# Kernel optimization log

Hardware: AMD Instinct MI355X
Metric: run time of the kernel (lower is better)

## Reference

```python
import jax, jax.numpy as jnp
import numpy as np
from jax import lax

DN = ('NCHW', 'OIHW', 'NCHW')

def conv(x, w, b, stride=1, pad=0):
    y = lax.conv_general_dilated(x, w, (stride, stride), ((pad, pad), (pad, pad)), dimension_numbers=DN)
    return y + b[None, :, None, None]

def conv_transpose(x, w, b):
    # torch ConvTranspose2d(k=4, s=2, p=1): w is (in_ch, out_ch, 4, 4)
    wf = jnp.flip(w, (2, 3)).transpose(1, 0, 2, 3)  # -> (out_ch, in_ch, 4, 4)
    pad = 4 - 1 - 1  # k - 1 - p = 2
    y = lax.conv_general_dilated(x, wf, (1, 1), ((pad, pad), (pad, pad)), lhs_dilation=(2, 2), dimension_numbers=DN)
    return y + b[None, :, None, None]

def setup_inputs() -> dict:
    key = jax.random.key(0)
    ks = jax.random.split(key, 16)
    HID, ZC, K = 256, 64, 512
    def w(k, shape):
        return (jax.random.normal(k, shape, jnp.float32) * 0.02)
    z = lambda n: jnp.zeros((n,), jnp.float32)
    return {
        'x': jax.random.uniform(ks[0], (8, 3, 128, 128), jnp.float32),
        'c1_w': w(ks[1], (HID, 3, 4, 4)), 'c1_b': z(HID),
        'c2_w': w(ks[2], (HID, HID, 4, 4)), 'c2_b': z(HID),
        'r0_w3': w(ks[3], (HID, HID, 3, 3)), 'r0_b3': z(HID),
        'r0_w1': w(ks[4], (HID, HID, 1, 1)), 'r0_b1': z(HID),
        'r1_w3': w(ks[5], (HID, HID, 3, 3)), 'r1_b3': z(HID),
        'r1_w1': w(ks[6], (HID, HID, 1, 1)), 'r1_b1': z(HID),
        'to_z_w': w(ks[7], (ZC, HID, 1, 1)), 'to_z_b': z(ZC),
        'codebook': jax.random.uniform(ks[8], (K, ZC), jnp.float32, -1.0 / K, 1.0 / K),
        'from_z_w': w(ks[9], (HID, ZC, 1, 1)), 'from_z_b': z(HID),
        't1_w': w(ks[10], (HID, HID, 4, 4)), 't1_b': z(HID),
        't2_w': w(ks[11], (HID, 3, 4, 4)), 't2_b': z(3),
    }

def _vqvae(x, c1_w, c1_b, c2_w, c2_b, r0_w3, r0_b3, r0_w1, r0_b1,
           r1_w3, r1_b3, r1_w1, r1_b1, to_z_w, to_z_b, codebook,
           from_z_w, from_z_b, t1_w, t1_b, t2_w, t2_b):
    # ---- Encoder ----
    h = jax.nn.relu(conv(x, c1_w, c1_b, stride=2, pad=1))
    h = jax.nn.relu(conv(h, c2_w, c2_b, stride=2, pad=1))
    for (w3, b3, w1, b1) in ((r0_w3, r0_b3, r0_w1, r0_b1), (r1_w3, r1_b3, r1_w1, r1_b1)):
        r = conv(jax.nn.relu(h), w3, b3, pad=1)
        r = conv(jax.nn.relu(r), w1, b1)
        h = h + r
    z_e = conv(h, to_z_w, to_z_b)  # [B, ZC, H/4, W/4]
    # ---- Vector quantization ----
    B, C, H, W = z_e.shape
    z_flat = z_e.transpose(0, 2, 3, 1).reshape(-1, C)  # [N, C]
    dist = (jnp.sum(z_flat * z_flat, axis=1, keepdims=True)
            - 2.0 * z_flat @ codebook.T
            + jnp.sum(codebook * codebook, axis=1)[None, :])  # [N, K]
    ids = jnp.argmin(dist, axis=1)  # [N]
    e_k_flat = codebook[ids]  # [N, C]
    e_k_st_flat = z_flat + lax.stop_gradient(e_k_flat - z_flat)
    e_k = e_k_flat.reshape(B, H, W, C).transpose(0, 3, 1, 2)
    e_k_st = e_k_st_flat.reshape(B, H, W, C).transpose(0, 3, 1, 2)
    ids = ids.reshape(B, H, W)
    # ---- Decoder ----
    d = jax.nn.relu(conv(e_k_st, from_z_w, from_z_b))
    d = jax.nn.relu(conv_transpose(d, t1_w, t1_b))
    out = jax.nn.sigmoid(conv_transpose(d, t2_w, t2_b))
    return out, z_e, e_k, ids

def reference(x, c1_w, c1_b, c2_w, c2_b, r0_w3, r0_b3, r0_w1, r0_b1,
              r1_w3, r1_b3, r1_w1, r1_b1, to_z_w, to_z_b, codebook,
              from_z_w, from_z_b, t1_w, t1_b, t2_w, t2_b):
    return _vqvae(x, c1_w, c1_b, c2_w, c2_b, r0_w3, r0_b3, r0_w1, r0_b1,
                  r1_w3, r1_b3, r1_w1, r1_b1, to_z_w, to_z_b, codebook,
                  from_z_w, from_z_b, t1_w, t1_b, t2_w, t2_b)
```

## Files before the change

kernel.cpp:

```cpp
#include <hip/hip_runtime.h>
#include <math.h>


typedef unsigned int uint;
typedef unsigned short ushort_t;
using short8 = __attribute__((ext_vector_type(8))) short;
using f32x4  = __attribute__((ext_vector_type(4))) float;

__device__ __attribute__((aligned(16))) ushort_t g_zpad[512];

static __device__ __forceinline__ int rfl(int x) { return __builtin_amdgcn_readfirstlane(x); }
static __device__ __forceinline__ ushort_t f2bf(float f) {
  uint u = __float_as_uint(f);
  return (ushort_t)((u + 0x7fffu + ((u >> 16) & 1u)) >> 16);
}
static __device__ __forceinline__ float bf2f(ushort_t b) {
  return __uint_as_float(((uint)b) << 16);
}
static __device__ __forceinline__ void gload16(const ushort_t* g, void* l) {
  __builtin_amdgcn_global_load_lds(
      (const __attribute__((address_space(1))) void*)g,
      (__attribute__((address_space(3))) void*)l, 16, 0, 0);
}

__global__ __launch_bounds__(256) void k_prep_misc(
    const float* __restrict__ c1w, float* __restrict__ wt_c1,
    const float* __restrict__ tozw, float* __restrict__ wt_toz,
    const float* __restrict__ fromzw, float* __restrict__ wt_fromz,
    const float* __restrict__ cb, float* __restrict__ cnorm,
    const float* __restrict__ t2w, ushort_t* __restrict__ w2pk)
{
  const int b = blockIdx.x, tid = threadIdx.x;
  if (b < 48) {
    int idx = b * 256 + tid;
    int co = idx % 256, i = idx / 256;
    wt_c1[idx] = c1w[co * 48 + i];
  } else if (b < 112) {
    int idx = (b - 48) * 256 + tid;
    int co = idx % 64, i = idx / 64;
    wt_toz[idx] = tozw[co * 256 + i];
  } else if (b < 176) {
    int idx = (b - 112) * 256 + tid;
    int co = idx % 256, i = idx / 256;
    wt_fromz[idx] = fromzw[co * 64 + i];
  } else if (b < 178) {
    int idx = (b - 176) * 256 + tid;
    if (idx < 512) {
      float s = 0.f;
      for (int c = 0; c < 64; ++c) { float v = cb[idx * 64 + c]; s = fmaf(v, v, s); }
      cnorm[idx] = s;
    }
  } else {
    int idx = (b - 178) * 256 + tid;
    int k = idx & 31, co = (idx >> 5) & 15, chunk = (idx >> 9) & 31, par = idx >> 14;
    int tap = chunk >> 3, cg = chunk & 7;
    int a = tap >> 1, bb = tap & 1;
    int ry = par & 1, rx = (par >> 1) & 1;
    int ky = ((ry + 1) & 1) + 2 * a;
    int kx = ((rx + 1) & 1) + 2 * bb;
    int ci = cg * 32 + k;
    float v = (co < 3) ? t2w[((ci * 3 + co) << 4) + ky * 4 + kx] : 0.f;
    w2pk[idx] = f2bf(v);
  }
}

template<int KIND>
__global__ __launch_bounds__(256) void k_prep_enc(
    const float* __restrict__ w, ushort_t* __restrict__ wp)
{
  constexpr int KK = (KIND == 0) ? 16 : (KIND == 1 ? 9 : 1);
  constexpr int KW = (KIND == 0) ? 4  : (KIND == 1 ? 3 : 1);
  constexpr int NT = KK;
  const int tid = threadIdx.x;
  const int wvg = blockIdx.x * 4 + (tid >> 6);
  const int lane = tid & 63;
  const int co = wvg >> 2;
  const int ci = (wvg & 3) * 64 + lane;
  const float* src = w + (size_t)(co * 256 + ci) * KK;
  const int coT = co >> 6, row = co & 63, cg = ci >> 5, k = ci & 31;
  float v[KK];
#pragma unroll
  for (int j = 0; j < KK; ++j) v[j] = src[j];
#pragma unroll
  for (int tap = 0; tap < NT; ++tap) {
    int ky, kx;
    if (KIND == 0)      { ky = tap >> 2; kx = tap & 3; }
    else if (KIND == 1) { ky = tap / 3;  kx = tap - ky * 3; }
    else                { ky = 0; kx = 0; }
    float val = v[ky * KW + kx];
    ushort_t b0 = f2bf(val);
    ushort_t b1 = f2bf(val - bf2f(b0));
    const int chunk = tap * 8 + cg;
    size_t base = ((size_t)(chunk * 4 + coT) << 12) + row * 32 + k;
    wp[base] = b0;
    wp[base + 2048] = b1;
  }
}

template<int KIND>
__global__ __launch_bounds__(256) void k_prep_enc2(
    const float* __restrict__ wa, ushort_t* __restrict__ oa,
    const float* __restrict__ wb2, ushort_t* __restrict__ ob)
{
  constexpr int KK = (KIND == 0) ? 16 : (KIND == 1 ? 9 : 1);
  constexpr int KW = (KIND == 0) ? 4  : (KIND == 1 ? 3 : 1);
  constexpr int NT = KK;
  const float* w = (blockIdx.x < 256) ? wa : wb2;
  ushort_t* wp = (blockIdx.x < 256) ? oa : ob;
  const int bx = blockIdx.x & 255;
  const int tid = threadIdx.x;
  const int wvg = bx * 4 + (tid >> 6);
  const int lane = tid & 63;
  const int co = wvg >> 2;
  const int ci = (wvg & 3) * 64 + lane;
  const float* src = w + (size_t)(co * 256 + ci) * KK;
  const int coT = co >> 6, row = co & 63, cg = ci >> 5, k = ci & 31;
  float v[KK];
#pragma unroll
  for (int j = 0; j < KK; ++j) v[j] = src[j];
#pragma unroll
  for (int tap = 0; tap < NT; ++tap) {
    int ky, kx;
    if (KIND == 0)      { ky = tap >> 2; kx = tap & 3; }
    else if (KIND == 1) { ky = tap / 3;  kx = tap - ky * 3; }
    else                { ky = 0; kx = 0; }
    float val = v[ky * KW + kx];
    ushort_t b0 = f2bf(val);
    ushort_t b1 = f2bf(val - bf2f(b0));
    const int chunk = tap * 8 + cg;
    size_t base = ((size_t)(chunk * 4 + coT) << 12) + row * 32 + k;
    wp[base] = b0;
    wp[base + 2048] = b1;
  }
}

__global__ void k_prep_t1w(const float* __restrict__ w, ushort_t* __restrict__ wb) {
  int idx = blockIdx.x * 256 + threadIdx.x;
  int kk  = idx & 31;
  int co  = (idx >> 5) & 255;
  int c8  = (idx >> 13) & 7;
  int tap = (idx >> 16) & 3;
  int par = idx >> 18;
  int ry = par & 1, rx = (par >> 1) & 1;
  int a = tap >> 1, b = tap & 1;
  int ky = ((ry + 1) & 1) + 2 * a;
  int kx = ((rx + 1) & 1) + 2 * b;
  int ci = c8 * 32 + kk;
  wb[idx] = f2bf(w[((ci * 256 + co) << 4) + ky * 4 + kx]);
}

__global__ __launch_bounds__(256) void k_conv1_split(
    const float* __restrict__ in, ushort_t* __restrict__ o0, ushort_t* __restrict__ o1,
    const float* __restrict__ wT, const float* __restrict__ bias)
{
  __shared__ float s_in[3 * 360];
  const int tid = threadIdx.x;
  const int lane = tid & 63;
  const int wv = rfl(tid >> 6);
  const int px = lane & 7, py = lane >> 3;
  const int tx = blockIdx.x & 7, ty = blockIdx.x >> 3;
  const int X = tx * 8, Y = ty * 8;
  const int cob = blockIdx.y * 64 + wv * 16;
  const int n = blockIdx.z;
  float acc[16];
#pragma unroll
  for (int i = 0; i < 16; ++i) acc[i] = bias[cob + i];
  const float* inN = in + (size_t)n * 3 * 16384;
  for (int e = tid; e < 3 * 360; e += 256) {
    int col2 = e % 20; int t = e / 20; int row = t % 18; int ci = t / 18;
    int pr = col2 / 10, hc = col2 % 10, ixl = 2 * hc + pr;
    int iy = 2 * Y - 1 + row, ix = 2 * X - 1 + ixl;
    float v = 0.f;
    if (ixl < 18 && (unsigned)iy < 128u && (unsigned)ix < 128u)
      v = inN[ci * 16384 + iy * 128 + ix];
    s_in[e] = v;
  }
  __syncthreads();
  const float* wc = wT + cob;
#pragma unroll
  for (int c = 0; c < 3; ++c) {
    const float* base = s_in + c * 360 + py * 40 + px;
#pragma unroll
    for (int ky = 0; ky < 4; ++ky) {
#pragma unroll
      for (int kx = 0; kx < 4; ++kx) {
        float iv = base[ky * 20 + (kx & 1) * 10 + (kx >> 1)];
        const float* w = wc + (size_t)(c * 16 + ky * 4 + kx) * 256;
#pragma unroll
        for (int i = 0; i < 16; ++i) acc[i] = fmaf(iv, w[i], acc[i]);
      }
    }
  }
  const int pxg = n * 4096 + (Y + py) * 64 + (X + px);
  uint p0[8], p1[8];
#pragma unroll
  for (int i = 0; i < 8; ++i) {
    float va = fmaxf(acc[2 * i], 0.f), vb = fmaxf(acc[2 * i + 1], 0.f);
    ushort_t a0 = f2bf(va), b0 = f2bf(vb);
    ushort_t a1 = f2bf(va - bf2f(a0)), b1 = f2bf(vb - bf2f(b0));
    p0[i] = (uint)a0 | ((uint)b0 << 16);
    p1[i] = (uint)a1 | ((uint)b1 << 16);
  }
  ushort_t* d0 = o0 + (size_t)pxg * 256 + cob;
  ushort_t* d1 = o1 + (size_t)pxg * 256 + cob;
  uint4 v0a; v0a.x = p0[0]; v0a.y = p0[1]; v0a.z = p0[2]; v0a.w = p0[3];
  uint4 v0b; v0b.x = p0[4]; v0b.y = p0[5]; v0b.z = p0[6]; v0b.w = p0[7];
  uint4 v1a; v1a.x = p1[0]; v1a.y = p1[1]; v1a.z = p1[2]; v1a.w = p1[3];
  uint4 v1b; v1b.x = p1[4]; v1b.y = p1[5]; v1b.z = p1[6]; v1b.w = p1[7];
  *(uint4*)d0 = v0a; *(uint4*)(d0 + 8) = v0b;
  *(uint4*)d1 = v1a; *(uint4*)(d1 + 8) = v1b;
}

template<int KIND>
__global__ __launch_bounds__(256) void k_enc_mfma_split(
    const ushort_t* __restrict__ x0, const ushort_t* __restrict__ x1,
    const ushort_t* __restrict__ wp, float* __restrict__ part)
{
  __shared__ ushort_t smem[2][12288];
  const int tid = threadIdx.x, lane = tid & 63, wv = tid >> 6;
  const int l15 = lane & 15, q = lane >> 4;
  const int pxT = blockIdx.x, coT = blockIdx.y;
  constexpr int NCH = (KIND == 0) ? 128 : 72;
  const int CH0 = blockIdx.z * (NCH / 2), CH1 = CH0 + NCH / 2;
  f32x4 acc[4][2];
#pragma unroll
  for (int m = 0; m < 4; ++m)
#pragma unroll
    for (int n = 0; n < 2; ++n) acc[m][n] = (f32x4){0.f, 0.f, 0.f, 0.f};

  const int r0 = tid >> 2, kq = tid & 3;
  int bimg[2], bu[2], bvc[2];
#pragma unroll
  for (int r = 0; r < 2; ++r) {
    int bpx = pxT * 128 + r0 + r * 64;
    bimg[r] = bpx >> 10; int bp = bpx & 1023; bu[r] = bp >> 5; bvc[r] = bp & 31;
  }
  const ushort_t* srcB[2][2];
  int ptap = -1;
  auto retap = [&](int tap) {
    ptap = tap;
    int ky, kx;
    if (KIND == 0) { ky = tap >> 2; kx = tap & 3; }
    else           { ky = tap / 3;  kx = tap - ky * 3; }
#pragma unroll
    for (int r = 0; r < 2; ++r) {
      bool v; size_t rowb;
      if (KIND == 0) {
        int iy = 2 * bu[r] - 1 + ky, ix = 2 * bvc[r] - 1 + kx;
        v = ((unsigned)iy < 64u) && ((unsigned)ix < 64u);
        rowb = ((size_t)(bimg[r] * 4096 + iy * 64 + ix)) << 8;
      } else {
        int iy = bu[r] - 1 + ky, ix = bvc[r] - 1 + kx;
        v = ((unsigned)iy < 32u) && ((unsigned)ix < 32u);
        rowb = ((size_t)(bimg[r] * 1024 + iy * 32 + ix)) << 8;
      }
      srcB[r][0] = (v ? (x0 + rowb) : g_zpad) + kq * 8;
      srcB[r][1] = (v ? (x1 + rowb) : g_zpad) + kq * 8;
    }
  };

  const int wvb = wv * 1024;
  auto stage = [&](int chunk, int bi) {
    const int tap = chunk >> 3, cg = chunk & 7;
    if (tap != ptap) retap(tap);
    char* bufb = (char*)smem[bi];
    const ushort_t* ap = wp + ((size_t)(chunk * 4 + coT) << 12) + tid * 8;
    gload16(ap,        bufb + wvb);
    gload16(ap + 2048, bufb + 4096 + wvb);
    const int ko = cg * 32;
    gload16(srcB[0][0] + ko, bufb + 8192 + wvb);
    gload16(srcB[1][0] + ko, bufb + 8192 + 4096 + wvb);
    gload16(srcB[0][1] + ko, bufb + 16384 + wvb);
    gload16(srcB[1][1] + ko, bufb + 16384 + 4096 + wvb);
  };
  auto compute = [&](const ushort_t* buf) {
    const ushort_t* sA = buf;
    const ushort_t* sB = buf + 4096;
    short8 af[4][2], bf[2][2];
#pragma unroll
    for (int m = 0; m < 4; ++m)
#pragma unroll
      for (int pl = 0; pl < 2; ++pl)
        af[m][pl] = *(const short8*)(sA + pl * 2048 + (m * 16 + l15) * 32 + q * 8);
#pragma unroll
    for (int n = 0; n < 2; ++n)
#pragma unroll
      for (int pl = 0; pl < 2; ++pl)
        bf[n][pl] = *(const short8*)(sB + pl * 4096 + (wv * 32 + n * 16 + l15) * 32 + q * 8);
#pragma unroll
    for (int m = 0; m < 4; ++m)
#pragma unroll
      for (int n = 0; n < 2; ++n) {
        acc[m][n] = __builtin_amdgcn_mfma_f32_16x16x32_bf16(af[m][0], bf[n][0], acc[m][n], 0, 0, 0);
        acc[m][n] = __builtin_amdgcn_mfma_f32_16x16x32_bf16(af[m][0], bf[n][1], acc[m][n], 0, 0, 0);
        acc[m][n] = __builtin_amdgcn_mfma_f32_16x16x32_bf16(af[m][1], bf[n][0], acc[m][n], 0, 0, 0);
      }
  };

  stage(CH0, 0);
  __syncthreads();
  int cur = 0;
  for (int c = CH0; c < CH1; ++c) {
    if (c + 1 < CH1) stage(c + 1, cur ^ 1);
    compute(smem[cur]);
    __syncthreads();
    cur ^= 1;
  }

  float* pz = part + ((size_t)blockIdx.z << 21);
#pragma unroll
  for (int m = 0; m < 4; ++m) {
#pragma unroll
    for (int n = 0; n < 2; ++n) {
#pragma unroll
      for (int r = 0; r < 4; ++r) {
        const int co_l = m * 16 + q * 4 + r;
        const int px_l = wv * 32 + n * 16 + l15;
        const int px = pxT * 128 + px_l;
        const int img = px >> 10, pp = px & 1023;
        const size_t ha = ((size_t)(img * 256 + coT * 64 + co_l)) * 1024 + pp;
        pz[ha] = acc[m][n][r];
      }
    }
  }
}

__global__ __launch_bounds__(256) void k_enc_mfma_3x3h(
    const ushort_t* __restrict__ x0, const ushort_t* __restrict__ x1,
    const ushort_t* __restrict__ wp, float* __restrict__ part)
{
  __shared__ ushort_t smem[32768];
  const int tid = threadIdx.x, lane = tid & 63, wv = tid >> 6;
  const int l15 = lane & 15, q = lane >> 4;
  const int pxT = blockIdx.x, coT = blockIdx.y;
  const int CG0 = blockIdx.z * 4;
  const int img = pxT >> 3;
  const int U0 = (pxT & 7) * 4;
  f32x4 acc[2][2];
#pragma unroll
  for (int m = 0; m < 2; ++m)
#pragma unroll
    for (int n = 0; n < 2; ++n) acc[m][n] = (f32x4){0.f, 0.f, 0.f, 0.f};

  const ushort_t* srcp[7];
#pragma unroll
  for (int i = 0; i < 7; ++i) {
    int slot = i * 256 + tid;
    int pl = slot >= 816 ? 1 : 0;
    int rem = slot - pl * 816;
    int rr = rem / 136;
    int c4 = rem - rr * 136;
    int cc = c4 >> 2, kq2 = c4 & 3;
    int iy = U0 - 1 + rr, ix = cc - 1;
    bool valid = (slot < 1632) && ((unsigned)iy < 32u) && ((unsigned)ix < 32u);
    const ushort_t* base = valid
        ? ((pl ? x1 : x0) + (((size_t)(img * 1024 + iy * 32 + ix)) << 8))
        : g_zpad;
    srcp[i] = base + kq2 * 8;
  }
  const int apl = tid >> 7;
  const int aus = apl * 2048 + (coT & 1) * 1024 + (tid & 127) * 8;
  const int coTq = coT >> 1;
  const int wvb = wv * 1024;
  char* bufb = (char*)smem;

  for (int cg = CG0; cg < CG0 + 4; ++cg) {
#pragma unroll
    for (int tap = 0; tap < 9; ++tap) {
      const int chunk = tap * 8 + cg;
      gload16(wp + ((size_t)(chunk * 4 + coTq) << 12) + aus, bufb + tap * 4096 + wvb);
    }
    const int ko = cg * 32;
#pragma unroll
    for (int i = 0; i < 7; ++i)
      gload16(srcp[i] + ko, bufb + 36864 + i * 4096 + wvb);
    __syncthreads();
    const ushort_t* Ab = smem;
    const ushort_t* Hb = smem + 18432;
#pragma unroll 3
    for (int tap = 0; tap < 9; ++tap) {
      const int ky = tap / 3, kx = tap - ky * 3;
      short8 af[2][2], bf[2][2];
#pragma unroll
      for (int m = 0; m < 2; ++m)
#pragma unroll
        for (int pl = 0; pl < 2; ++pl)
          af[m][pl] = *(const short8*)(Ab + tap * 2048 + pl * 1024 + (m * 16 + l15) * 32 + q * 8);
      const int r = wv + ky;
#pragma unroll
      for (int n = 0; n < 2; ++n)
#pragma unroll
        for (int pl = 0; pl < 2; ++pl)
          bf[n][pl] = *(const short8*)(Hb + pl * 6528 + r * 1088 + (n * 16 + l15 + kx) * 32 + q * 8);
#pragma unroll
      for (int m = 0; m < 2; ++m)
#pragma unroll
        for (int n = 0; n < 2; ++n) {
          acc[m][n] = __builtin_amdgcn_mfma_f32_16x16x32_bf16(af[m][0], bf[n][0], acc[m][n], 0, 0, 0);
          acc[m][n] = __builtin_amdgcn_mfma_f32_16x16x32_bf16(af[m][0], bf[n][1], acc[m][n], 0, 0, 0);
          acc[m][n] = __builtin_amdgcn_mfma_f32_16x16x32_bf16(af[m][1], bf[n][0], acc[m][n], 0, 0, 0);
        }
    }
    __syncthreads();
  }

  float* pz = part + ((size_t)blockIdx.z << 21);
#pragma unroll
  for (int m = 0; m < 2; ++m) {
#pragma unroll
    for (int n = 0; n < 2; ++n) {
#pragma unroll
      for (int r = 0; r < 4; ++r) {
        const int co_l = m * 16 + q * 4 + r;
        const int px_l = wv * 32 + n * 16 + l15;
        const int px = pxT * 128 + px_l;
        const int imgp = px >> 10, pp = px & 1023;
        const size_t ha = ((size_t)(imgp * 256 + coT * 32 + co_l)) * 1024 + pp;
        pz[ha] = acc[m][n][r];
      }
    }
  }
}

template<bool WH>
__global__ __launch_bounds__(256) void k_enc_epi(
    const float* __restrict__ part, float* __restrict__ h32,
    ushort_t* __restrict__ s0, ushort_t* __restrict__ s1,
    const float* __restrict__ bias)
{
  const int px = blockIdx.x * 256 + threadIdx.x;
  const int co0 = blockIdx.y * 16;
  const int img = px >> 10, pp = px & 1023;
  const float* part1 = part + (1u << 21);
  uint p0[8], p1[8];
#pragma unroll
  for (int i = 0; i < 8; ++i) {
    size_t ha = ((size_t)(img * 256 + co0 + 2 * i)) * 1024 + pp;
    size_t hb = ha + 1024;
    float va = part[ha] + part1[ha] + bias[co0 + 2 * i];
    float vb = part[hb] + part1[hb] + bias[co0 + 2 * i + 1];
    float sa, sb;
    if (WH) {
      va = fmaxf(va, 0.f); vb = fmaxf(vb, 0.f);
      h32[ha] = va; h32[hb] = vb; sa = va; sb = vb;
    } else { sa = fmaxf(va, 0.f); sb = fmaxf(vb, 0.f); }
    ushort_t a0 = f2bf(sa), b0 = f2bf(sb);
    p0[i] = (uint)a0 | ((uint)b0 << 16);
    p1[i] = (uint)f2bf(sa - bf2f(a0)) | ((uint)f2bf(sb - bf2f(b0)) << 16);
  }
  ushort_t* d0 = s0 + (size_t)px * 256 + co0;
  ushort_t* d1 = s1 + (size_t)px * 256 + co0;
  uint4 v0a; v0a.x = p0[0]; v0a.y = p0[1]; v0a.z = p0[2]; v0a.w = p0[3];
  uint4 v0b; v0b.x = p0[4]; v0b.y = p0[5]; v0b.z = p0[6]; v0b.w = p0[7];
  uint4 v1a; v1a.x = p1[0]; v1a.y = p1[1]; v1a.z = p1[2]; v1a.w = p1[3];
  uint4 v1b; v1b.x = p1[4]; v1b.y = p1[5]; v1b.z = p1[6]; v1b.w = p1[7];
  *(uint4*)d0 = v0a; *(uint4*)(d0 + 8) = v0b;
  *(uint4*)d1 = v1a; *(uint4*)(d1 + 8) = v1b;
}

template<bool WS>
__global__ __launch_bounds__(256) void k_enc_mfma(
    const ushort_t* __restrict__ x0, const ushort_t* __restrict__ x1,
    const ushort_t* __restrict__ wp, const float* __restrict__ bias,
    float* __restrict__ h32, ushort_t* __restrict__ sp0, ushort_t* __restrict__ sp1)
{
  __shared__ ushort_t smem[24576];
  const int tid = threadIdx.x, lane = tid & 63, wv = tid >> 6;
  const int l15 = lane & 15, q = lane >> 4;
  const int pxT = blockIdx.x, coT = blockIdx.y;
  f32x4 acc[4][2];
#pragma unroll
  for (int m = 0; m < 4; ++m)
#pragma unroll
    for (int n = 0; n < 2; ++n) acc[m][n] = (f32x4){0.f, 0.f, 0.f, 0.f};

  const int r0 = tid >> 2, kq = tid & 3;
  const ushort_t* srcB[2][2];
#pragma unroll
  for (int r = 0; r < 2; ++r) {
    size_t rowb = ((size_t)(pxT * 128 + r0 + r * 64)) << 8;
    srcB[r][0] = x0 + rowb + kq * 8;
    srcB[r][1] = x1 + rowb + kq * 8;
  }
  const int wvb = wv * 1024;
  auto stage = [&](int c, int bi) {
    char* bufb = (char*)(smem + bi * 12288);
    const ushort_t* ap = wp + ((size_t)(c * 4 + coT) << 12) + tid * 8;
    gload16(ap,        bufb + wvb);
    gload16(ap + 2048, bufb + 4096 + wvb);
    const int ko = c * 32;
    gload16(srcB[0][0] + ko, bufb + 8192 + wvb);
    gload16(srcB[1][0] + ko, bufb + 8192 + 4096 + wvb);
    gload16(srcB[0][1] + ko, bufb + 16384 + wvb);
    gload16(srcB[1][1] + ko, bufb + 16384 + 4096 + wvb);
  };
  auto compute = [&](const ushort_t* buf) {
    const ushort_t* sA = buf;
    const ushort_t* sB = buf + 4096;
    short8 af[4][2], bf[2][2];
#pragma unroll
    for (int m = 0; m < 4; ++m)
#pragma unroll
      for (int pl = 0; pl < 2; ++pl)
        af[m][pl] = *(const short8*)(sA + pl * 2048 + (m * 16 + l15) * 32 + q * 8);
#pragma unroll
    for (int n = 0; n < 2; ++n)
#pragma unroll
      for (int pl = 0; pl < 2; ++pl)
        bf[n][pl] = *(const short8*)(sB + pl * 4096 + (wv * 32 + n * 16 + l15) * 32 + q * 8);
#pragma unroll
    for (int m = 0; m < 4; ++m)
#pragma unroll
      for (int n = 0; n < 2; ++n) {
        acc[m][n] = __builtin_amdgcn_mfma_f32_16x16x32_bf16(af[m][0], bf[n][0], acc[m][n], 0, 0, 0);
        acc[m][n] = __builtin_amdgcn_mfma_f32_16x16x32_bf16(af[m][0], bf[n][1], acc[m][n], 0, 0, 0);
        acc[m][n] = __builtin_amdgcn_mfma_f32_16x16x32_bf16(af[m][1], bf[n][0], acc[m][n], 0, 0, 0);
      }
  };

  stage(0, 0);
  __syncthreads();
  int cur = 0;
  for (int c = 0; c < 8; ++c) {
    if (c + 1 < 8) stage(c + 1, cur ^ 1);
    compute(smem + cur * 12288);
    __syncthreads();
    cur ^= 1;
  }

#pragma unroll
  for (int m = 0; m < 4; ++m) {
#pragma unroll
    for (int n = 0; n < 2; ++n) {
#pragma unroll
      for (int r = 0; r < 4; ++r) {
        const int co_l = m * 16 + q * 4 + r;
        const int px_l = wv * 32 + n * 16 + l15;
        float v = acc[m][n][r] + bias[coT * 64 + co_l];
        const int px = pxT * 128 + px_l;
        const int img = px >> 10, pp = px & 1023;
        const size_t ha = ((size_t)(img * 256 + coT * 64 + co_l)) * 1024 + pp;
        v += h32[ha];
        h32[ha] = v;
        if (WS) {
          float sv = fmaxf(v, 0.f);
          ushort_t b0 = f2bf(sv);
          smem[px_l * 72 + co_l] = b0;
          smem[9216 + px_l * 72 + co_l] = f2bf(sv - bf2f(b0));
        }
      }
    }
  }
  if (WS) {
    __syncthreads();
#pragma unroll
    for (int i = 0; i < 8; ++i) {
      int idx = tid + 256 * i;
      int pl = idx >> 10, w2 = idx & 1023, pxl = w2 >> 3, g = w2 & 7;
      uint4 vv = *(const uint4*)(smem + pl * 9216 + pxl * 72 + g * 8);
      ushort_t* dst = (pl ? sp1 : sp0) + ((size_t)(pxT * 128 + pxl)) * 256 + coT * 64 + g * 8;
      *(uint4*)dst = vv;
    }
  }
}

__global__ __launch_bounds__(256) void k_conv1x1(
    const float* __restrict__ in, float* __restrict__ out,
    const float* __restrict__ wT, const float* __restrict__ bias,
    int CI, int CO, int P)
{
  const int p = blockIdx.x * 256 + threadIdx.x;
  const int cob = blockIdx.y * 16;
  const int n = blockIdx.z;
  const float* inN = in + (size_t)n * CI * P + p;
  float acc[16];
#pragma unroll
  for (int i = 0; i < 16; ++i) acc[i] = bias[cob + i];
  const float* wr = wT + cob;
#pragma unroll 4
  for (int ci = 0; ci < CI; ++ci) {
    float iv = inN[(size_t)ci * P];
    const float* w = wr + (size_t)ci * CO;
#pragma unroll
    for (int i = 0; i < 16; ++i) acc[i] = fmaf(iv, w[i], acc[i]);
  }
  float* outN = out + (size_t)n * CO * P + p;
#pragma unroll
  for (int i = 0; i < 16; ++i) outN[(size_t)(cob + i) * P] = acc[i];
}

__global__ __launch_bounds__(256) void k_vq_part(
    const float* __restrict__ z_e, const float* __restrict__ cb,
    const float* __restrict__ cnorm, float* __restrict__ pbest, int* __restrict__ pbid)
{
  int g = blockIdx.x * 256 + threadIdx.x;
  int chunk = blockIdx.y;
  int img = g >> 10, p = g & 1023;
  const float* zp = z_e + (size_t)img * 64 * 1024 + p;
  float z[64];
#pragma unroll
  for (int c = 0; c < 64; ++c) z[c] = zp[(size_t)c * 1024];
  float best = 3.4e38f; int bid = chunk << 5;
  const int j0 = chunk << 5;
  for (int j = j0; j < j0 + 32; ++j) {
    const float* cj = cb + j * 64;
    float m = 0.f;
#pragma unroll
    for (int c = 0; c < 64; ++c) m = fmaf(z[c], cj[c], m);
    float d = fmaf(-2.f, m, cnorm[j]);
    if (d < best) { best = d; bid = j; }
  }
  pbest[chunk * 8192 + g] = best;
  pbid[chunk * 8192 + g] = bid;
}

__global__ __launch_bounds__(256) void k_vq_reduce(
    const float* __restrict__ pbest, const int* __restrict__ pbid,
    const float* __restrict__ cb, float* __restrict__ ids_f, float* __restrict__ ek)
{
  int g = blockIdx.x * 256 + threadIdx.x;
  float best = 3.4e38f; int bid = 0;
#pragma unroll
  for (int ch = 0; ch < 16; ++ch) {
    float d = pbest[ch * 8192 + g];
    int b = pbid[ch * 8192 + g];
    if (d < best) { best = d; bid = b; }
  }
  ids_f[g] = (float)bid;
  int img = g >> 10, p = g & 1023;
  const float* cbid = cb + bid * 64;
  float* ekp = ek + (size_t)img * 64 * 1024 + p;
#pragma unroll
  for (int c = 0; c < 64; ++c) ekp[(size_t)c * 1024] = cbid[c];
}

__global__ __launch_bounds__(256) void k_from_z(
    const float* __restrict__ ek, ushort_t* __restrict__ nhwc,
    const float* __restrict__ wT, const float* __restrict__ bias)
{
  const int p = blockIdx.x * 256 + threadIdx.x;
  const int co0 = blockIdx.y * 16;
  const int n = blockIdx.z;
  const float* inN = ek + (size_t)n * 64 * 1024 + p;
  float acc[16];
#pragma unroll
  for (int i = 0; i < 16; ++i) acc[i] = bias[co0 + i];
#pragma unroll 4
  for (int ci = 0; ci < 64; ++ci) {
    float iv = inN[(size_t)ci * 1024];
    const float* w = wT + (size_t)ci * 256 + co0;
#pragma unroll
    for (int i = 0; i < 16; ++i) acc[i] = fmaf(iv, w[i], acc[i]);
  }
  uint pk[8];
#pragma unroll
  for (int i = 0; i < 8; ++i) {
    ushort_t lo = f2bf(fmaxf(acc[2 * i], 0.f));
    ushort_t hi = f2bf(fmaxf(acc[2 * i + 1], 0.f));
    pk[i] = (uint)lo | ((uint)hi << 16);
  }
  ushort_t* op = nhwc + (((size_t)n * 1024 + p) * 256 + co0);
  uint4 v0; v0.x = pk[0]; v0.y = pk[1]; v0.z = pk[2]; v0.w = pk[3];
  uint4 v1; v1.x = pk[4]; v1.y = pk[5]; v1.z = pk[6]; v1.w = pk[7];
  *(uint4*)(op) = v0;
  *(uint4*)(op + 8) = v1;
}

__global__ __launch_bounds__(256) void k_mfma_t1(
    const ushort_t* __restrict__ nhwc, const ushort_t* __restrict__ wb,
    const float* __restrict__ bias, ushort_t* __restrict__ t1o)
{
  __shared__ ushort_t smem[24576];
  const int tid = threadIdx.x;
  const int lane = tid & 63;
  const int wv = tid >> 6;
  const int wm = wv & 1, wn = wv >> 1;
  const int l15 = lane & 15, q = lane >> 4;
  const int pxT = blockIdx.x, coT = blockIdx.y, par = blockIdx.z;
  const int ry = par & 1, rx = (par >> 1) & 1;
  const int pxbase = pxT * 128;
  const int img = pxbase >> 10;
  const int U0 = (pxT & 7) * 4;
  f32x4 acc[4][4];
#pragma unroll
  for (int i = 0; i < 4; ++i)
#pragma unroll
    for (int j = 0; j < 4; ++j) acc[i][j] = (f32x4){0.f, 0.f, 0.f, 0.f};

  const ushort_t* srcp[4];
#pragma unroll
  for (int i = 0; i < 4; ++i) {
    int slot = i * 256 + tid;
    int rr = slot / 136;
    int c4 = slot - rr * 136;
    int cc = c4 >> 2, kq2 = c4 & 3;
    int iy = U0 - 1 + rr, ix = cc - 1;
    bool valid = (slot < 816) && ((unsigned)iy < 32u) && ((unsigned)ix < 32u);
    const ushort_t* base = valid
        ? (nhwc + (((size_t)(img * 1024 + iy * 32 + ix)) << 8))
        : g_zpad;
    srcp[i] = base + kq2 * 8;
  }
  const int wvb = wv * 1024;
  char* bufb = (char*)smem;

  for (int c8 = 0; c8 < 8; ++c8) {
#pragma unroll
    for (int tap = 0; tap < 4; ++tap) {
      const ushort_t* Ab = wb + ((size_t)((par * 4 + tap) * 8 + c8) << 13)
                           + coT * 4096 + tid * 8;
      gload16(Ab,        bufb + tap * 8192 + wvb);
      gload16(Ab + 2048, bufb + tap * 8192 + 4096 + wvb);
    }
    const int ko = c8 * 32;
#pragma unroll
    for (int i = 0; i < 4; ++i)
      gload16(srcp[i] + ko, bufb + 32768 + i * 4096 + wvb);
    __syncthreads();
    const ushort_t* A = smem;
    const ushort_t* H = smem + 16384;
#pragma unroll
    for (int tap = 0; tap < 4; ++tap) {
      const int a = tap >> 1, b = tap & 1;
      const int dr = ry + 1 - a, dc = rx + 1 - b;
      short8 af[4], bfr[4];
#pragma unroll
      for (int i = 0; i < 4; ++i)
        af[i] = *(const short8*)(A + tap * 4096 + (wm * 64 + i * 16 + l15) * 32 + q * 8);
#pragma unroll
      for (int j = 0; j < 4; ++j) {
        const int row = wn * 64 + j * 16 + l15;
        const int rr = (row >> 5) + dr, cc = (row & 31) + dc;
        bfr[j] = *(const short8*)(H + rr * 1088 + cc * 32 + q * 8);
      }
#pragma unroll
      for (int i = 0; i < 4; ++i)
#pragma unroll
        for (int j = 0; j < 4; ++j)
          acc[i][j] = __builtin_amdgcn_mfma_f32_16x16x32_bf16(af[i], bfr[j], acc[i][j], 0, 0, 0);
    }
    __syncthreads();
  }

#pragma unroll
  for (int i = 0; i < 4; ++i) {
    int co = coT * 128 + wm * 64 + i * 16 + q * 4;
#pragma unroll
    for (int j = 0; j < 4; ++j) {
      int px = pxbase + wn * 64 + j * 16 + l15;
      int u = (px >> 5) & 31, vv = px & 31;
      int oy = 2 * u + ry, ox = 2 * vv + rx;
      ushort_t e0 = f2bf(fmaxf(acc[i][j][0] + bias[co + 0], 0.f));
      ushort_t e1 = f2bf(fmaxf(acc[i][j][1] + bias[co + 1], 0.f));
      ushort_t e2 = f2bf(fmaxf(acc[i][j][2] + bias[co + 2], 0.f));
      ushort_t e3 = f2bf(fmaxf(acc[i][j][3] + bias[co + 3], 0.f));
      uint2 pk; pk.x = (uint)e0 | ((uint)e1 << 16); pk.y = (uint)e2 | ((uint)e3 << 16);
      *(uint2*)(t1o + ((size_t)(img * 4096 + oy * 64 + ox) * 256 + co)) = pk;
    }
  }
}

__global__ __launch_bounds__(256) void k_mfma_t2(
    const ushort_t* __restrict__ t1o, const ushort_t* __restrict__ wb,
    const float* __restrict__ bias, float* __restrict__ out)
{
  __shared__ ushort_t smem[2][8704];
  const int tid = threadIdx.x, lane = tid & 63, wv = tid >> 6;
  const int l15 = lane & 15, q = lane >> 4;
  const int pxb = blockIdx.x * 256;
  const int par = blockIdx.y;
  const int ry = par & 1, rx = (par >> 1) & 1;
  f32x4 acc[4];
#pragma unroll
  for (int m = 0; m < 4; ++m) acc[m] = (f32x4){0.f, 0.f, 0.f, 0.f};
  const int kg = tid & 3;
  const ushort_t* srcA[4];
  int ptap = -1;
  auto retap = [&](int tap) {
    ptap = tap;
    const int a = tap >> 1, b = tap & 1;
#pragma unroll
    for (int i = 0; i < 4; ++i) {
      int row = (tid >> 2) + 64 * i;
      int px = pxb + row;
      int img = px >> 12, p = px & 4095, u = p >> 6, v = p & 63;
      int iy = u + ry - a, ix = v + rx - b;
      bool valid = ((unsigned)iy < 64u) && ((unsigned)ix < 64u);
      srcA[i] = (valid ? (t1o + (((size_t)(img * 4096 + iy * 64 + ix)) << 8)) : g_zpad)
                + kg * 8;
    }
  };
  const int wvb = wv * 1024;
  auto stage = [&](int c, int bi) {
    const int tap = c >> 3, cg = c & 7;
    if (tap != ptap) retap(tap);
    char* bufb = (char*)smem[bi];
    const int ko = cg * 32;
#pragma unroll
    for (int i = 0; i < 4; ++i)
      gload16(srcA[i] + ko, bufb + i * 4096 + wvb);
    if (tid < 64)
      gload16(wb + ((size_t)(par * 32 + c)) * 512 + tid * 8, bufb + 16384);
  };
  auto compute = [&](const ushort_t* buf) {
    const ushort_t* sA = buf;
    const ushort_t* sB = buf + 8192;
    short8 bf = *(const short8*)(sB + l15 * 32 + q * 8);
#pragma unroll
    for (int m = 0; m < 4; ++m) {
      const int row = wv * 64 + m * 16 + l15;
      short8 af = *(const short8*)(sA + row * 32 + q * 8);
      acc[m] = __builtin_amdgcn_mfma_f32_16x16x32_bf16(af, bf, acc[m], 0, 0, 0);
    }
  };

  stage(0, 0);
  __syncthreads();
  int cur = 0;
  for (int c = 0; c < 32; ++c) {
    if (c + 1 < 32) stage(c + 1, cur ^ 1);
    compute(smem[cur]);
    __syncthreads();
    cur ^= 1;
  }

  const int co = l15;
  if (co < 3) {
    float bco = bias[co];
#pragma unroll
    for (int m = 0; m < 4; ++m) {
#pragma unroll
      for (int r = 0; r < 4; ++r) {
        int px = pxb + wv * 64 + m * 16 + q * 4 + r;
        int img = px >> 12, p = px & 4095, u = p >> 6, v = p & 63;
        size_t addr = ((size_t)(img * 3 + co)) * 16384 + (2 * u + ry) * 128 + (2 * v + rx);
        out[addr] = 1.f / (1.f + expf(-(acc[m][r] + bco)));
      }
    }
  }
}

extern "C" void kernel_launch(void* const* d_in, const int* in_sizes, int n_in,
                              void* d_out, int out_size, void* d_ws, size_t ws_size,
                              hipStream_t stream) {
  (void)in_sizes; (void)n_in; (void)out_size; (void)ws_size;
  const float* x      = (const float*)d_in[0];
  const float* c1_w   = (const float*)d_in[1];
  const float* c1_b   = (const float*)d_in[2];
  const float* c2_w   = (const float*)d_in[3];
  const float* c2_b   = (const float*)d_in[4];
  const float* r0_w3  = (const float*)d_in[5];
  const float* r0_b3  = (const float*)d_in[6];
  const float* r0_w1  = (const float*)d_in[7];
  const float* r0_b1  = (const float*)d_in[8];
  const float* r1_w3  = (const float*)d_in[9];
  const float* r1_b3  = (const float*)d_in[10];
  const float* r1_w1  = (const float*)d_in[11];
  const float* r1_b1  = (const float*)d_in[12];
  const float* to_z_w = (const float*)d_in[13];
  const float* to_z_b = (const float*)d_in[14];
  const float* cb     = (const float*)d_in[15];
  const float* from_z_w = (const float*)d_in[16];
  const float* from_z_b = (const float*)d_in[17];
  const float* t1_w   = (const float*)d_in[18];
  const float* t1_b   = (const float*)d_in[19];
  const float* t2_w   = (const float*)d_in[20];
  const float* t2_b   = (const float*)d_in[21];

  float* wsf = (float*)d_ws;
  ushort_t* xs1p0 = (ushort_t*)(wsf + 0);
  ushort_t* xs1p1 = (ushort_t*)(wsf + 4194304);
  float*    cp0   = wsf + 8388608;
  float*    h32   = wsf + 8388608;
  float*    qp0   = wsf + 4194304;
  ushort_t* sE0   = (ushort_t*)(wsf + 0);
  ushort_t* sE1   = (ushort_t*)(wsf + 1048576);
  ushort_t* sF0   = (ushort_t*)(wsf + 2097152);
  ushort_t* sF1   = (ushort_t*)(wsf + 3145728);
  float*    pbest = wsf + 0;
  int*      pbid  = (int*)(wsf + 131072);
  ushort_t* t1out = (ushort_t*)(wsf + 2097152);
  ushort_t* decn  = (ushort_t*)(wsf + 6291456);
  ushort_t* wp_c2   = (ushort_t*)(wsf + 12582912);
  ushort_t* wp_r0w3 = (ushort_t*)(wsf + 13631488);
  ushort_t* wp_r1w3 = (ushort_t*)(wsf + 14221312);
  ushort_t* wp_r0w1 = (ushort_t*)(wsf + 14811136);
  ushort_t* wp_r1w1 = (ushort_t*)(wsf + 14876672);
  float*    wt_c1   = wsf + 14942208;
  float*    wt_toz  = wsf + 14954496;
  float*    wt_fromz= wsf + 14970880;
  ushort_t* t1wb    = (ushort_t*)(wsf + 14987264);
  ushort_t* w2pk    = (ushort_t*)(wsf + 15511552);
  float*    cnorm   = wsf + 15544320;

  float* out_img = (float*)d_out;
  float* z_e_out = out_img + 393216;
  float* e_k_out = z_e_out + 524288;
  float* ids_out = e_k_out + 524288;

  k_prep_misc<<<434, 256, 0, stream>>>(c1_w, wt_c1, to_z_w, wt_toz,
                                       from_z_w, wt_fromz, cb, cnorm, t2_w, w2pk);
  k_prep_enc<0><<<256, 256, 0, stream>>>(c2_w, wp_c2);
  k_prep_enc2<1><<<512, 256, 0, stream>>>(r0_w3, wp_r0w3, r1_w3, wp_r1w3);
  k_prep_enc2<2><<<512, 256, 0, stream>>>(r0_w1, wp_r0w1, r1_w1, wp_r1w1);
  k_prep_t1w<<<4096, 256, 0, stream>>>(t1_w, t1wb);

  k_conv1_split<<<dim3(64, 4, 8), 256, 0, stream>>>(x, xs1p0, xs1p1, wt_c1, c1_b);
  k_enc_mfma_split<0><<<dim3(64, 4, 2), 256, 0, stream>>>(xs1p0, xs1p1, wp_c2, cp0);
  k_enc_epi<true><<<dim3(32, 16), 256, 0, stream>>>(cp0, h32, sE0, sE1, c2_b);
  k_enc_mfma_3x3h<<<dim3(64, 8, 2), 256, 0, stream>>>(sE0, sE1, wp_r0w3, qp0);
  k_enc_epi<false><<<dim3(32, 16), 256, 0, stream>>>(qp0, nullptr, sE0, sE1, r0_b3);
  k_enc_mfma<true ><<<dim3(64, 4), 256, 0, stream>>>(
      sE0, sE1, wp_r0w1, r0_b1, h32, sF0, sF1);
  k_enc_mfma_3x3h<<<dim3(64, 8, 2), 256, 0, stream>>>(sF0, sF1, wp_r1w3, qp0);
  k_enc_epi<false><<<dim3(32, 16), 256, 0, stream>>>(qp0, nullptr, sE0, sE1, r1_b3);
  k_enc_mfma<false><<<dim3(64, 4), 256, 0, stream>>>(
      sE0, sE1, wp_r1w1, r1_b1, h32, nullptr, nullptr);
  k_conv1x1<<<dim3(4, 4, 8), 256, 0, stream>>>(h32, z_e_out, wt_toz, to_z_b, 256, 64, 1024);

  k_vq_part<<<dim3(32, 16), 256, 0, stream>>>(z_e_out, cb, cnorm, pbest, pbid);
  k_vq_reduce<<<32, 256, 0, stream>>>(pbest, pbid, cb, ids_out, e_k_out);

  k_from_z<<<dim3(4, 16, 8), 256, 0, stream>>>(e_k_out, decn, wt_fromz, from_z_b);
  k_mfma_t1<<<dim3(64, 2, 4), 256, 0, stream>>>(decn, t1wb, t1_b, t1out);
  k_mfma_t2<<<dim3(128, 4), 256, 0, stream>>>(t1out, w2pk, t2_b, out_img);
}
```

Baseline: 403.3 us.

## Fuse 3x3 residual conv epilogue into MFMA kernel, drop split-K partials

New measurement: 392.2 us. 1.03x faster.

```diff
diff --git a/kernel.cpp b/kernel.cpp
--- a/kernel.cpp
+++ b/kernel.cpp
@@ -325,15 +325,15 @@
   }
 }
 
-__global__ __launch_bounds__(256) void k_enc_mfma_3x3h(
+__global__ __launch_bounds__(256) void k_enc_mfma_3x3f(
     const ushort_t* __restrict__ x0, const ushort_t* __restrict__ x1,
-    const ushort_t* __restrict__ wp, float* __restrict__ part)
+    const ushort_t* __restrict__ wp, const float* __restrict__ bias,
+    ushort_t* __restrict__ s0, ushort_t* __restrict__ s1)
 {
   __shared__ ushort_t smem[32768];
   const int tid = threadIdx.x, lane = tid & 63, wv = tid >> 6;
   const int l15 = lane & 15, q = lane >> 4;
   const int pxT = blockIdx.x, coT = blockIdx.y;
-  const int CG0 = blockIdx.z * 4;
   const int img = pxT >> 3;
   const int U0 = (pxT & 7) * 4;
   f32x4 acc[2][2];
@@ -364,7 +364,7 @@
   const int wvb = wv * 1024;
   char* bufb = (char*)smem;
 
-  for (int cg = CG0; cg < CG0 + 4; ++cg) {
+  for (int cg = 0; cg < 8; ++cg) {
 #pragma unroll
     for (int tap = 0; tap < 9; ++tap) {
       const int chunk = tap * 8 + cg;
@@ -404,7 +404,7 @@
     __syncthreads();
   }
 
-  float* pz = part + ((size_t)blockIdx.z << 21);
+  const int cob = coT * 32;
 #pragma unroll
   for (int m = 0; m < 2; ++m) {
 #pragma unroll
@@ -413,12 +413,23 @@
       for (int r = 0; r < 4; ++r) {
         const int co_l = m * 16 + q * 4 + r;
         const int px_l = wv * 32 + n * 16 + l15;
-        const int px = pxT * 128 + px_l;
-        const int imgp = px >> 10, pp = px & 1023;
-        const size_t ha = ((size_t)(imgp * 256 + coT * 32 + co_l)) * 1024 + pp;
-        pz[ha] = acc[m][n][r];
+        float sv = fmaxf(acc[m][n][r] + bias[cob + co_l], 0.f);
+        ushort_t b0 = f2bf(sv);
+        smem[px_l * 32 + co_l] = b0;
+        smem[4096 + px_l * 32 + co_l] = f2bf(sv - bf2f(b0));
       }
     }
+  }
+  __syncthreads();
+#pragma unroll
+  for (int i = 0; i < 4; ++i) {
+    int idx = tid + 256 * i;
+    int pl = idx >> 9;
+    int rem = idx & 511;
+    int px_l = rem >> 2, g = rem & 3;
+    uint4 vv = *(const uint4*)(smem + pl * 4096 + px_l * 32 + g * 8);
+    ushort_t* dst = (pl ? s1 : s0) + ((size_t)(pxT * 128 + px_l)) * 256 + cob + g * 8;
+    *(uint4*)dst = vv;
   }
 }
 
@@ -872,7 +883,6 @@
   ushort_t* xs1p1 = (ushort_t*)(wsf + 4194304);
   float*    cp0   = wsf + 8388608;
   float*    h32   = wsf + 8388608;
-  float*    qp0   = wsf + 4194304;
   ushort_t* sE0   = (ushort_t*)(wsf + 0);
   ushort_t* sE1   = (ushort_t*)(wsf + 1048576);
   ushort_t* sF0   = (ushort_t*)(wsf + 2097152);
@@ -908,14 +918,12 @@
   k_conv1_split<<<dim3(64, 4, 8), 256, 0, stream>>>(x, xs1p0, xs1p1, wt_c1, c1_b);
   k_enc_mfma_split<0><<<dim3(64, 4, 2), 256, 0, stream>>>(xs1p0, xs1p1, wp_c2, cp0);
   k_enc_epi<true><<<dim3(32, 16), 256, 0, stream>>>(cp0, h32, sE0, sE1, c2_b);
-  k_enc_mfma_3x3h<<<dim3(64, 8, 2), 256, 0, stream>>>(sE0, sE1, wp_r0w3, qp0);
-  k_enc_epi<false><<<dim3(32, 16), 256, 0, stream>>>(qp0, nullptr, sE0, sE1, r0_b3);
+  k_enc_mfma_3x3f<<<dim3(64, 8), 256, 0, stream>>>(sE0, sE1, wp_r0w3, r0_b3, sF0, sF1);
   k_enc_mfma<true ><<<dim3(64, 4), 256, 0, stream>>>(
-      sE0, sE1, wp_r0w1, r0_b1, h32, sF0, sF1);
-  k_enc_mfma_3x3h<<<dim3(64, 8, 2), 256, 0, stream>>>(sF0, sF1, wp_r1w3, qp0);
-  k_enc_epi<false><<<dim3(32, 16), 256, 0, stream>>>(qp0, nullptr, sE0, sE1, r1_b3);
+      sF0, sF1, wp_r0w1, r0_b1, h32, sE0, sE1);
+  k_enc_mfma_3x3f<<<dim3(64, 8), 256, 0, stream>>>(sE0, sE1, wp_r1w3, r1_b3, sF0, sF1);
   k_enc_mfma<false><<<dim3(64, 4), 256, 0, stream>>>(
-      sE0, sE1, wp_r1w1, r1_b1, h32, nullptr, nullptr);
+      sF0, sF1, wp_r1w1, r1_b1, h32, nullptr, nullptr);
   k_conv1x1<<<dim3(4, 4, 8), 256, 0, stream>>>(h32, z_e_out, wt_toz, to_z_b, 256, 64, 1024);
 
   k_vq_part<<<dim3(32, 16), 256, 0, stream>>>(z_e_out, cb, cnorm, pbest, pbid);
```
